# Performance work log

Hardware: AMD Instinct MI355X
Metric: run time of the kernel (lower is better)

The kernel has to match this reference:

```python
import jax, jax.numpy as jnp
import numpy as np

N = 65536          # number of active voxels
GRID = 96          # sparse volume side
P = 4              # cardinality (paths)
KS = 3             # kernel size per dim
K = KS ** 3        # 27 kernel offsets
DILS = [1, 3, 9, 27]
C_IN = 128
C_PATH = 32        # in/out features per path = 128 / 4
BN_EPS = 1e-5
LEAK = 0.0


def _build_kernel_maps():
    """Build padded gather/scatter maps per (path, kernel offset).

    in_map[p,k,:] / out_map[p,k,:]: out[out_idx] += W[k] @ x[in_idx].
    Padded with sentinel index N (maps to a zero row / dumped row).
    """
    rng = np.random.default_rng(0)
    flat = rng.choice(GRID ** 3, size=N, replace=False)
    coords = np.stack(np.unravel_index(flat, (GRID, GRID, GRID)), axis=1)  # [N,3]
    order = np.argsort(flat)
    sorted_keys = flat[order]
    offs = np.array([[dx, dy, dz] for dx in (-1, 0, 1)
                     for dy in (-1, 0, 1) for dz in (-1, 0, 1)])
    in_map = np.full((P, K, N), N, dtype=np.int32)
    out_map = np.full((P, K, N), N, dtype=np.int32)
    for p in range(P):
        d = DILS[p]
        for k in range(K):
            nb = coords + offs[k] * d
            valid = np.all((nb >= 0) & (nb < GRID), axis=1)
            nbkey = nb[:, 0] * GRID * GRID + nb[:, 1] * GRID + nb[:, 2]
            pos = np.clip(np.searchsorted(sorted_keys, nbkey), 0, N - 1)
            hit = valid & (sorted_keys[pos] == nbkey)
            j = np.nonzero(hit)[0]
            in_map[p, k, :j.size] = order[pos[j]].astype(np.int32)
            out_map[p, k, :j.size] = j.astype(np.int32)
    return jnp.asarray(in_map), jnp.asarray(out_map)


def setup_inputs() -> dict:
    key = jax.random.key(0)
    ks = jax.random.split(key, 4)
    in_map, out_map = _build_kernel_maps()
    return {
        "feats": jax.random.normal(ks[0], (N, C_IN), jnp.float32),
        "lin_W": jax.random.normal(ks[1], (P, C_IN, C_PATH), jnp.float32) * 0.05,
        "lin_b": jnp.zeros((P, C_PATH), jnp.float32),
        "conv_W": jax.random.normal(ks[2], (P, K, C_PATH, C_PATH), jnp.float32) * 0.05,
        "gamma": jnp.ones((P, C_PATH), jnp.float32),
        "beta": jnp.zeros((P, C_PATH), jnp.float32),
        "fin_W": jax.random.normal(ks[3], (C_IN, C_IN), jnp.float32) * 0.05,
        "fin_b": jnp.zeros((C_IN,), jnp.float32),
        "in_map": in_map,
        "out_map": out_map,
    }


def _sparse_conv(x, W, im, om):
    """x: [N,C]; W: [K,C,Co]; im/om: [K,N] padded index maps."""
    n = x.shape[0]
    co = W.shape[2]
    xp = jnp.concatenate([x, jnp.zeros((1, x.shape[1]), x.dtype)], axis=0)
    gathered = xp[im]                                   # [K,N,C]
    contrib = jnp.einsum('knc,kcd->knd', gathered, W)   # [K,N,Co]
    out = jnp.zeros((n + 1, co), x.dtype)
    out = out.at[om.reshape(-1)].add(contrib.reshape(-1, co))
    return out[:n]


def reference(feats, lin_W, lin_b, conv_W, gamma, beta, fin_W, fin_b,
              in_map, out_map):
    outs = []
    for p in range(P):
        h = feats @ lin_W[p] + lin_b[p]                 # MinkowskiLinear
        h = _sparse_conv(h, conv_W[p], in_map[p], out_map[p])
        mu = h.mean(axis=0)                             # BN (training stats)
        var = h.var(axis=0)
        h = (h - mu) * jax.lax.rsqrt(var + BN_EPS) * gamma[p] + beta[p]
        h = jax.nn.leaky_relu(h, LEAK)
        outs.append(h)
    cat = jnp.concatenate(outs, axis=1)                 # [N, 128]
    out = cat @ fin_W + fin_b + feats                   # linear + residual (identity)
    return out
```

## Files before the change

### kernel.cpp

```cpp
#include <hip/hip_runtime.h>


#define NN    65536
#define CIN   128
#define CPATH 32
#define NPATH 4
#define NK    27
#define TJ    512
#define NTILE (NN / TJ)
#define MAXG  288
#define SCALE_F 2097152.0f
#define INV_SCALE 4.76837158203125e-7f

typedef __attribute__((ext_vector_type(8))) short bfx8;
typedef __attribute__((ext_vector_type(4))) float fx4;

__device__ __forceinline__ unsigned short f2bf(float f) {
    unsigned u = __builtin_bit_cast(unsigned, f);
    u += 0x7FFFu + ((u >> 16) & 1u);
    return (unsigned short)(u >> 16);
}
__device__ __forceinline__ float bf2f(unsigned short s) {
    return __builtin_bit_cast(float, (unsigned)s << 16);
}
__device__ __forceinline__ bfx8 pack_bf8(const float4 a, const float4 b) {
    union { unsigned short s[8]; bfx8 v; } u;
    u.s[0] = f2bf(a.x); u.s[1] = f2bf(a.y); u.s[2] = f2bf(a.z); u.s[3] = f2bf(a.w);
    u.s[4] = f2bf(b.x); u.s[5] = f2bf(b.y); u.s[6] = f2bf(b.z); u.s[7] = f2bf(b.w);
    return u.v;
}

__global__ void wprep_rng(const float* __restrict__ convW,
                          const float* __restrict__ linW,
                          const float* __restrict__ finW,
                          const int* __restrict__ om,
                          unsigned short* __restrict__ Wt,
                          unsigned short* __restrict__ Wlt,
                          unsigned short* __restrict__ Wft,
                          unsigned short* __restrict__ Hb,
                          int* __restrict__ rngAll) {
    const int b = blockIdx.x;
    const int t = threadIdx.x;
    if (b < 108) {
        if (b == 0 && t < 64)
            ((unsigned*)(Hb + (size_t)NN * CIN))[t] = 0u;
        const int m = t >> 3;
        const int c0 = (t & 7) * 4;
        const float4 w = *(const float4*)(convW + ((size_t)b * CPATH + m) * CPATH + c0);
        unsigned short* o = Wt + (size_t)b * CPATH * CPATH;
        o[(c0 + 0) * CPATH + m] = f2bf(w.x);
        o[(c0 + 1) * CPATH + m] = f2bf(w.y);
        o[(c0 + 2) * CPATH + m] = f2bf(w.z);
        o[(c0 + 3) * CPATH + m] = f2bf(w.w);
    } else if (b < 112) {
        const int col = (b - 108) * 32 + (t >> 3);
        const int p = col >> 5, c = col & 31;
        const int k0 = (t & 7) * 16;
        for (int k = k0; k < k0 + 16; k++)
            Wlt[col * CIN + k] = f2bf(linW[(size_t)p * CIN * CPATH + k * CPATH + c]);
    } else if (b < 116) {
        const int col = (b - 112) * 32 + (t >> 3);
        const int k0 = (t & 7) * 16;
        for (int k = k0; k < k0 + 16; k++)
            Wft[col * CIN + k] = f2bf(finW[(size_t)k * CIN + col]);
    } else {
        const int idx = (b - 116) * 256 + t;
        if (idx < NPATH * NK * (NTILE + 1)) {
            const int tile = idx % (NTILE + 1);
            const int pk = idx / (NTILE + 1);
            const int bound = tile * TJ;
            const int* o = om + (size_t)pk * NN;
            int lo = 0, hi = NN;
            while (lo < hi) {
                const int mid = (lo + hi) >> 1;
                if (o[mid] < bound) lo = mid + 1; else hi = mid;
            }
            rngAll[idx] = lo;
        }
    }
}

__global__ void __launch_bounds__(256, 4)
lin_mfma(const float* __restrict__ feats,
         const unsigned short* __restrict__ Wlt,
         const float* __restrict__ linb,
         unsigned short* __restrict__ Hb) {
    const int tid = threadIdx.x;
    const int w = tid >> 6, lane = tid & 63;
    const int mrow = lane & 15, kq = lane >> 4;
    const int row = blockIdx.x * 64 + w * 16 + mrow;

    fx4 acc[8];
#pragma unroll
    for (int g = 0; g < 8; g++) acc[g] = (fx4){0.f, 0.f, 0.f, 0.f};

#pragma unroll
    for (int kt = 0; kt < 4; ++kt) {
        const float4 y0 = *(const float4*)(feats + (size_t)row * CIN + kt * 32 + kq * 8);
        const float4 y1 = *(const float4*)(feats + (size_t)row * CIN + kt * 32 + kq * 8 + 4);
        const bfx8 yf = pack_bf8(y0, y1);
#pragma unroll
        for (int g = 0; g < 8; g++) {
            const bfx8 xf = *(const bfx8*)(Wlt + (size_t)(g * 16 + mrow) * CIN + kt * 32 + kq * 8);
            acc[g] = __builtin_amdgcn_mfma_f32_16x16x32_bf16(xf, yf, acc[g], 0, 0, 0);
        }
    }
#pragma unroll
    for (int g = 0; g < 8; g++) {
        const int c0 = g * 16 + kq * 4;
        const float4 bb = *(const float4*)(linb + c0);
        union { unsigned short s[4]; ushort4 v; } u;
        u.s[0] = f2bf(acc[g][0] + bb.x);
        u.s[1] = f2bf(acc[g][1] + bb.y);
        u.s[2] = f2bf(acc[g][2] + bb.z);
        u.s[3] = f2bf(acc[g][3] + bb.w);
        *(ushort4*)(Hb + (size_t)row * CIN + c0) = u.v;
    }
}

__global__ void __launch_bounds__(512)
sconv12(const unsigned short* __restrict__ Hb,
        const unsigned short* __restrict__ Wt,
        const int* __restrict__ im,
        const int* __restrict__ om,
        const int* __restrict__ rngAll,
        unsigned short* __restrict__ Cbh,
        float* __restrict__ part) {
    __shared__ int accI[TJ + 1][33];
    __shared__ int rng[NK][2];
    __shared__ int gkA[MAXG], gtA[MAXG];
    __shared__ int gbase[NK];
    __shared__ int Gs;
    __shared__ float redS[16][32], redQ[16][32];

    const int p = blockIdx.y;
    const int T = blockIdx.x;
    const int j0 = T * TJ;
    const int tid = threadIdx.x;
    const int lane = tid & 63;
    const int w = tid >> 6;
    const int mrow = lane & 15, kq = lane >> 4;

    for (int idx = tid; idx < (TJ + 1) * 33; idx += 512)
        (&accI[0][0])[idx] = 0;
    if (tid < NK * 2) {
        const int k = tid >> 1, which = tid & 1;
        rng[k][which] = rngAll[((size_t)p * NK + k) * (NTILE + 1) + T + which];
    }
    __syncthreads();
    if (tid == 0) {
        int sum = 0;
#pragma unroll
        for (int k = 0; k < NK; k++) {
            gbase[k] = sum;
            sum += (rng[k][1] - rng[k][0] + 15) >> 4;
        }
        Gs = sum;
    }
    __syncthreads();
    if (tid < NK) {
        const int k = tid;
        const int s = rng[k][0];
        const int n = (rng[k][1] - s + 15) >> 4;
        const int b = gbase[k];
        for (int g = 0; g < n; g++) {
            gkA[b + g] = k;
            gtA[b + g] = s + g * 16;
        }
    }
    __syncthreads();

    const int G = Gs;
    const unsigned short* Wp = Wt + (size_t)p * NK * 1024 + kq * 8;
    const unsigned short* Hp = Hb + (size_t)p * CPATH + kq * 8;
    const int* omP = om + (size_t)p * NK * NN;
    const int* imP = im + (size_t)p * NK * NN;
    const fx4 z4 = {0.f, 0.f, 0.f, 0.f};

    for (int base = 2 * w; base < G; base += 16) {
        const int kA = gkA[base];
        const int tA = gtA[base] + mrow;
        int kB = 0, tB = NN + mrow;
        if (base + 1 < G) { kB = gkA[base + 1]; tB = gtA[base + 1] + mrow; }
        const int eA = rng[kA][1], eB = rng[kB][1];
        const bool vA = tA < eA, vB = tB < eB;
        const int jjA = vA ? (omP[(size_t)kA * NN + tA] - j0) : TJ;
        const int iA  = vA ? imP[(size_t)kA * NN + tA] : NN;
        const int jjB = vB ? (omP[(size_t)kB * NN + tB] - j0) : TJ;
        const int iB  = vB ? imP[(size_t)kB * NN + tB] : NN;
        const bfx8 xA0 = *(const bfx8*)(Wp + (size_t)kA * 1024 + mrow * CPATH);
        const bfx8 xA1 = *(const bfx8*)(Wp + (size_t)kA * 1024 + (16 + mrow) * CPATH);
        const bfx8 xB0 = *(const bfx8*)(Wp + (size_t)kB * 1024 + mrow * CPATH);
        const bfx8 xB1 = *(const bfx8*)(Wp + (size_t)kB * 1024 + (16 + mrow) * CPATH);
        const bfx8 yA = *(const bfx8*)(Hp + (size_t)iA * CIN);
        const bfx8 yB = *(const bfx8*)(Hp + (size_t)iB * CIN);
        const fx4 dA0 = __builtin_amdgcn_mfma_f32_16x16x32_bf16(xA0, yA, z4, 0, 0, 0);
        const fx4 dA1 = __builtin_amdgcn_mfma_f32_16x16x32_bf16(xA1, yA, z4, 0, 0, 0);
        const fx4 dB0 = __builtin_amdgcn_mfma_f32_16x16x32_bf16(xB0, yB, z4, 0, 0, 0);
        const fx4 dB1 = __builtin_amdgcn_mfma_f32_16x16x32_bf16(xB1, yB, z4, 0, 0, 0);
#pragma unroll
        for (int r = 0; r < 4; r++) {
            atomicAdd(&accI[jjA][kq * 4 + r],      (int)rintf(dA0[r] * SCALE_F));
            atomicAdd(&accI[jjA][16 + kq * 4 + r], (int)rintf(dA1[r] * SCALE_F));
            atomicAdd(&accI[jjB][kq * 4 + r],      (int)rintf(dB0[r] * SCALE_F));
            atomicAdd(&accI[jjB][16 + kq * 4 + r], (int)rintf(dB1[r] * SCALE_F));
        }
    }
    __syncthreads();

    {
        const int c = tid & 31;
        const int rg = tid >> 5;
        float s = 0.f, q = 0.f;
        for (int m = 0; m < TJ / 16; m++) {
            const int r = rg + 16 * m;
            const float f = (float)accI[r][c] * INV_SCALE;
            s += f;
            q = fmaf(f, f, q);
            Cbh[(size_t)(j0 + r) * CIN + p * CPATH + c] = f2bf(f);
        }
        redS[rg][c] = s;
        redQ[rg][c] = q;
    }
    __syncthreads();
    if (tid < 32) {
        float s = 0.f;
#pragma unroll
        for (int g = 0; g < 16; g++) s += redS[g][tid];
        part[(((size_t)p * NTILE) + T) * 64 + tid] = s;
    } else if (tid < 64) {
        const int c = tid - 32;
        float q = 0.f;
#pragma unroll
        for (int g = 0; g < 16; g++) q += redQ[g][c];
        part[(((size_t)p * NTILE) + T) * 64 + 32 + c] = q;
    }
}

__global__ void bn_stats2(const float* __restrict__ part,
                          const float* __restrict__ gamma,
                          const float* __restrict__ beta,
                          float* __restrict__ ss) {
    __shared__ float rs[4][128], rq[4][128];
    const int c = threadIdx.x & 127;
    const int ch = threadIdx.x >> 7;
    const int p = c >> 5, cc = c & 31;
    float s = 0.f, s2 = 0.f;
    for (int t = ch * (NTILE / 4); t < (ch + 1) * (NTILE / 4); t++) {
        s += part[(((size_t)p * NTILE) + t) * 64 + cc];
        s2 += part[(((size_t)p * NTILE) + t) * 64 + 32 + cc];
    }
    rs[ch][c] = s;
    rq[ch][c] = s2;
    __syncthreads();
    if (ch == 0) {
        s = rs[0][c] + rs[1][c] + rs[2][c] + rs[3][c];
        s2 = rq[0][c] + rq[1][c] + rq[2][c] + rq[3][c];
        const float mean = s * (1.f / NN);
        const float var = s2 * (1.f / NN) - mean * mean;
        const float sc = gamma[c] * rsqrtf(var + 1e-5f);
        ss[c] = sc;
        ss[128 + c] = beta[c] - mean * sc;
    }
}

__global__ void __launch_bounds__(256, 4)
fin_mfma(const unsigned short* __restrict__ Cbh,
         const float* __restrict__ ss,
         const unsigned short* __restrict__ Wft,
         const float* __restrict__ finb,
         const float* __restrict__ feats,
         float* __restrict__ out) {
    const int tid = threadIdx.x;
    const int w = tid >> 6, lane = tid & 63;
    const int mrow = lane & 15, kq = lane >> 4;
    const int row = blockIdx.x * 64 + w * 16 + mrow;

    fx4 acc[8];
#pragma unroll
    for (int g = 0; g < 8; g++) acc[g] = (fx4){0.f, 0.f, 0.f, 0.f};

#pragma unroll
    for (int kt = 0; kt < 4; ++kt) {
        const int k0 = kt * 32 + kq * 8;
        union { unsigned short s[8]; bfx8 v; } cb;
        cb.v = *(const bfx8*)(Cbh + (size_t)row * CIN + k0);
        const float4 sc0 = *(const float4*)(ss + k0);
        const float4 sc1 = *(const float4*)(ss + k0 + 4);
        const float4 sh0 = *(const float4*)(ss + 128 + k0);
        const float4 sh1 = *(const float4*)(ss + 128 + k0 + 4);
        float4 a, b;
        a.x = fmaxf(fmaf(bf2f(cb.s[0]), sc0.x, sh0.x), 0.f);
        a.y = fmaxf(fmaf(bf2f(cb.s[1]), sc0.y, sh0.y), 0.f);
        a.z = fmaxf(fmaf(bf2f(cb.s[2]), sc0.z, sh0.z), 0.f);
        a.w = fmaxf(fmaf(bf2f(cb.s[3]), sc0.w, sh0.w), 0.f);
        b.x = fmaxf(fmaf(bf2f(cb.s[4]), sc1.x, sh1.x), 0.f);
        b.y = fmaxf(fmaf(bf2f(cb.s[5]), sc1.y, sh1.y), 0.f);
        b.z = fmaxf(fmaf(bf2f(cb.s[6]), sc1.z, sh1.z), 0.f);
        b.w = fmaxf(fmaf(bf2f(cb.s[7]), sc1.w, sh1.w), 0.f);
        const bfx8 yf = pack_bf8(a, b);
#pragma unroll
        for (int g = 0; g < 8; g++) {
            const bfx8 xf = *(const bfx8*)(Wft + (size_t)(g * 16 + mrow) * CIN + kt * 32 + kq * 8);
            acc[g] = __builtin_amdgcn_mfma_f32_16x16x32_bf16(xf, yf, acc[g], 0, 0, 0);
        }
    }
#pragma unroll
    for (int g = 0; g < 8; g++) {
        const int c0 = g * 16 + kq * 4;
        const float4 fb = *(const float4*)(finb + c0);
        const float4 rs = *(const float4*)(feats + (size_t)row * CIN + c0);
        float4 o;
        o.x = acc[g][0] + fb.x + rs.x;
        o.y = acc[g][1] + fb.y + rs.y;
        o.z = acc[g][2] + fb.z + rs.z;
        o.w = acc[g][3] + fb.w + rs.w;
        *(float4*)(out + (size_t)row * CIN + c0) = o;
    }
}

extern "C" void kernel_launch(void* const* d_in, const int* in_sizes, int n_in,
                              void* d_out, int out_size, void* d_ws,
                              size_t ws_size, hipStream_t stream) {
    (void)in_sizes; (void)n_in; (void)out_size; (void)ws_size;
    const float* feats = (const float*)d_in[0];
    const float* linW  = (const float*)d_in[1];
    const float* linb  = (const float*)d_in[2];
    const float* convW = (const float*)d_in[3];
    const float* gamma = (const float*)d_in[4];
    const float* beta  = (const float*)d_in[5];
    const float* finW  = (const float*)d_in[6];
    const float* finb  = (const float*)d_in[7];
    const int*   im    = (const int*)d_in[8];
    const int*   om    = (const int*)d_in[9];
    float* out = (float*)d_out;

    char* ws = (char*)d_ws;
    unsigned short* Hb  = (unsigned short*)(ws);
    unsigned short* Cbh = (unsigned short*)(ws + 16781312);
    unsigned short* Wt  = (unsigned short*)(ws + 33558528);
    unsigned short* Wlt = (unsigned short*)(ws + 33779712);
    unsigned short* Wft = (unsigned short*)(ws + 33812480);
    int*   rngAll       = (int*)(ws + 33845248);
    float* part         = (float*)(ws + 33902592);
    float* ss           = (float*)(ws + 34033664);

    const int rng_total = NPATH * NK * (NTILE + 1);
    const int rng_blocks = (rng_total + 255) / 256;
    wprep_rng<<<116 + rng_blocks, 256, 0, stream>>>(convW, linW, finW, om,
                                                    Wt, Wlt, Wft, Hb, rngAll);
    lin_mfma<<<1024, 256, 0, stream>>>(feats, Wlt, linb, Hb);
    sconv12<<<dim3(NTILE, NPATH), 512, 0, stream>>>(Hb, Wt, im, om, rngAll, Cbh, part);
    bn_stats2<<<1, 512, 0, stream>>>(part, gamma, beta, ss);
    fin_mfma<<<1024, 256, 0, stream>>>(Cbh, ss, Wft, finb, feats, out);
}
```

Before: 93.68 us.

## Fuse all stages into one cooperative persistent kernel with grid syncs

Measured after the change: 327.5 us. +249.6%, slower.

```diff
diff --git a/kernel.cpp b/kernel.cpp
--- a/kernel.cpp
+++ b/kernel.cpp
@@ -1,4 +1,7 @@
 #include <hip/hip_runtime.h>
+#include <hip/hip_cooperative_groups.h>
+
+namespace cg = cooperative_groups;
 
 
 #define NN    65536
@@ -6,9 +9,9 @@
 #define CPATH 32
 #define NPATH 4
 #define NK    27
-#define TJ    512
+#define TJ    256
 #define NTILE (NN / TJ)
-#define MAXG  288
+#define MAXG  192
 #define SCALE_F 2097152.0f
 #define INV_SCALE 4.76837158203125e-7f
 
@@ -30,41 +33,36 @@
     return u.v;
 }
 
-__global__ void wprep_rng(const float* __restrict__ convW,
-                          const float* __restrict__ linW,
-                          const float* __restrict__ finW,
-                          const int* __restrict__ om,
-                          unsigned short* __restrict__ Wt,
-                          unsigned short* __restrict__ Wlt,
-                          unsigned short* __restrict__ Wft,
-                          unsigned short* __restrict__ Hb,
-                          int* __restrict__ rngAll) {
-    const int b = blockIdx.x;
-    const int t = threadIdx.x;
-    if (b < 108) {
-        if (b == 0 && t < 64)
-            ((unsigned*)(Hb + (size_t)NN * CIN))[t] = 0u;
-        const int m = t >> 3;
-        const int c0 = (t & 7) * 4;
-        const float4 w = *(const float4*)(convW + ((size_t)b * CPATH + m) * CPATH + c0);
-        unsigned short* o = Wt + (size_t)b * CPATH * CPATH;
-        o[(c0 + 0) * CPATH + m] = f2bf(w.x);
-        o[(c0 + 1) * CPATH + m] = f2bf(w.y);
-        o[(c0 + 2) * CPATH + m] = f2bf(w.z);
-        o[(c0 + 3) * CPATH + m] = f2bf(w.w);
-    } else if (b < 112) {
-        const int col = (b - 108) * 32 + (t >> 3);
+__device__ __forceinline__ void wprep_body(int vb, int vt,
+        const float* __restrict__ convW, const float* __restrict__ linW,
+        const float* __restrict__ finW, const int* __restrict__ om,
+        unsigned short* __restrict__ Wt, unsigned short* __restrict__ Wlt,
+        unsigned short* __restrict__ Wft, unsigned short* __restrict__ Hb,
+        int* __restrict__ rngAll) {
+    if (vb < 108) {
+        if (vb == 0 && vt < 64)
+            ((unsigned*)(Hb + (size_t)NN * CIN))[vt] = 0u;
+        const int m = vt >> 3;
+        const int c0 = (vt & 7) * 4;
+        const float4 wv = *(const float4*)(convW + ((size_t)vb * CPATH + m) * CPATH + c0);
+        unsigned short* o = Wt + (size_t)vb * CPATH * CPATH;
+        o[(c0 + 0) * CPATH + m] = f2bf(wv.x);
+        o[(c0 + 1) * CPATH + m] = f2bf(wv.y);
+        o[(c0 + 2) * CPATH + m] = f2bf(wv.z);
+        o[(c0 + 3) * CPATH + m] = f2bf(wv.w);
+    } else if (vb < 112) {
+        const int col = (vb - 108) * 32 + (vt >> 3);
         const int p = col >> 5, c = col & 31;
-        const int k0 = (t & 7) * 16;
+        const int k0 = (vt & 7) * 16;
         for (int k = k0; k < k0 + 16; k++)
             Wlt[col * CIN + k] = f2bf(linW[(size_t)p * CIN * CPATH + k * CPATH + c]);
-    } else if (b < 116) {
-        const int col = (b - 112) * 32 + (t >> 3);
-        const int k0 = (t & 7) * 16;
+    } else if (vb < 116) {
+        const int col = (vb - 112) * 32 + (vt >> 3);
+        const int k0 = (vt & 7) * 16;
         for (int k = k0; k < k0 + 16; k++)
             Wft[col * CIN + k] = f2bf(finW[(size_t)k * CIN + col]);
     } else {
-        const int idx = (b - 116) * 256 + t;
+        const int idx = (vb - 116) * 256 + vt;
         if (idx < NPATH * NK * (NTILE + 1)) {
             const int tile = idx % (NTILE + 1);
             const int pk = idx / (NTILE + 1);
@@ -80,20 +78,12 @@
     }
 }
 
-__global__ void __launch_bounds__(256, 4)
-lin_mfma(const float* __restrict__ feats,
-         const unsigned short* __restrict__ Wlt,
-         const float* __restrict__ linb,
-         unsigned short* __restrict__ Hb) {
-    const int tid = threadIdx.x;
-    const int w = tid >> 6, lane = tid & 63;
-    const int mrow = lane & 15, kq = lane >> 4;
-    const int row = blockIdx.x * 64 + w * 16 + mrow;
-
+__device__ __forceinline__ void lin_body(int row, int mrow, int kq,
+        const float* __restrict__ feats, const unsigned short* __restrict__ Wlt,
+        const float* __restrict__ linb, unsigned short* __restrict__ Hb) {
     fx4 acc[8];
 #pragma unroll
     for (int g = 0; g < 8; g++) acc[g] = (fx4){0.f, 0.f, 0.f, 0.f};
-
 #pragma unroll
     for (int kt = 0; kt < 4; ++kt) {
         const float4 y0 = *(const float4*)(feats + (size_t)row * CIN + kt * 32 + kq * 8);
@@ -118,168 +108,13 @@
     }
 }
 
-__global__ void __launch_bounds__(512)
-sconv12(const unsigned short* __restrict__ Hb,
-        const unsigned short* __restrict__ Wt,
-        const int* __restrict__ im,
-        const int* __restrict__ om,
-        const int* __restrict__ rngAll,
-        unsigned short* __restrict__ Cbh,
-        float* __restrict__ part) {
-    __shared__ int accI[TJ + 1][33];
-    __shared__ int rng[NK][2];
-    __shared__ int gkA[MAXG], gtA[MAXG];
-    __shared__ int gbase[NK];
-    __shared__ int Gs;
-    __shared__ float redS[16][32], redQ[16][32];
-
-    const int p = blockIdx.y;
-    const int T = blockIdx.x;
-    const int j0 = T * TJ;
-    const int tid = threadIdx.x;
-    const int lane = tid & 63;
-    const int w = tid >> 6;
-    const int mrow = lane & 15, kq = lane >> 4;
-
-    for (int idx = tid; idx < (TJ + 1) * 33; idx += 512)
-        (&accI[0][0])[idx] = 0;
-    if (tid < NK * 2) {
-        const int k = tid >> 1, which = tid & 1;
-        rng[k][which] = rngAll[((size_t)p * NK + k) * (NTILE + 1) + T + which];
-    }
-    __syncthreads();
-    if (tid == 0) {
-        int sum = 0;
-#pragma unroll
-        for (int k = 0; k < NK; k++) {
-            gbase[k] = sum;
-            sum += (rng[k][1] - rng[k][0] + 15) >> 4;
-        }
-        Gs = sum;
-    }
-    __syncthreads();
-    if (tid < NK) {
-        const int k = tid;
-        const int s = rng[k][0];
-        const int n = (rng[k][1] - s + 15) >> 4;
-        const int b = gbase[k];
-        for (int g = 0; g < n; g++) {
-            gkA[b + g] = k;
-            gtA[b + g] = s + g * 16;
-        }
-    }
-    __syncthreads();
-
-    const int G = Gs;
-    const unsigned short* Wp = Wt + (size_t)p * NK * 1024 + kq * 8;
-    const unsigned short* Hp = Hb + (size_t)p * CPATH + kq * 8;
-    const int* omP = om + (size_t)p * NK * NN;
-    const int* imP = im + (size_t)p * NK * NN;
-    const fx4 z4 = {0.f, 0.f, 0.f, 0.f};
-
-    for (int base = 2 * w; base < G; base += 16) {
-        const int kA = gkA[base];
-        const int tA = gtA[base] + mrow;
-        int kB = 0, tB = NN + mrow;
-        if (base + 1 < G) { kB = gkA[base + 1]; tB = gtA[base + 1] + mrow; }
-        const int eA = rng[kA][1], eB = rng[kB][1];
-        const bool vA = tA < eA, vB = tB < eB;
-        const int jjA = vA ? (omP[(size_t)kA * NN + tA] - j0) : TJ;
-        const int iA  = vA ? imP[(size_t)kA * NN + tA] : NN;
-        const int jjB = vB ? (omP[(size_t)kB * NN + tB] - j0) : TJ;
-        const int iB  = vB ? imP[(size_t)kB * NN + tB] : NN;
-        const bfx8 xA0 = *(const bfx8*)(Wp + (size_t)kA * 1024 + mrow * CPATH);
-        const bfx8 xA1 = *(const bfx8*)(Wp + (size_t)kA * 1024 + (16 + mrow) * CPATH);
-        const bfx8 xB0 = *(const bfx8*)(Wp + (size_t)kB * 1024 + mrow * CPATH);
-        const bfx8 xB1 = *(const bfx8*)(Wp + (size_t)kB * 1024 + (16 + mrow) * CPATH);
-        const bfx8 yA = *(const bfx8*)(Hp + (size_t)iA * CIN);
-        const bfx8 yB = *(const bfx8*)(Hp + (size_t)iB * CIN);
-        const fx4 dA0 = __builtin_amdgcn_mfma_f32_16x16x32_bf16(xA0, yA, z4, 0, 0, 0);
-        const fx4 dA1 = __builtin_amdgcn_mfma_f32_16x16x32_bf16(xA1, yA, z4, 0, 0, 0);
-        const fx4 dB0 = __builtin_amdgcn_mfma_f32_16x16x32_bf16(xB0, yB, z4, 0, 0, 0);
-        const fx4 dB1 = __builtin_amdgcn_mfma_f32_16x16x32_bf16(xB1, yB, z4, 0, 0, 0);
-#pragma unroll
-        for (int r = 0; r < 4; r++) {
-            atomicAdd(&accI[jjA][kq * 4 + r],      (int)rintf(dA0[r] * SCALE_F));
-            atomicAdd(&accI[jjA][16 + kq * 4 + r], (int)rintf(dA1[r] * SCALE_F));
-            atomicAdd(&accI[jjB][kq * 4 + r],      (int)rintf(dB0[r] * SCALE_F));
-            atomicAdd(&accI[jjB][16 + kq * 4 + r], (int)rintf(dB1[r] * SCALE_F));
-        }
-    }
-    __syncthreads();
-
-    {
-        const int c = tid & 31;
-        const int rg = tid >> 5;
-        float s = 0.f, q = 0.f;
-        for (int m = 0; m < TJ / 16; m++) {
-            const int r = rg + 16 * m;
-            const float f = (float)accI[r][c] * INV_SCALE;
-            s += f;
-            q = fmaf(f, f, q);
-            Cbh[(size_t)(j0 + r) * CIN + p * CPATH + c] = f2bf(f);
-        }
-        redS[rg][c] = s;
-        redQ[rg][c] = q;
-    }
-    __syncthreads();
-    if (tid < 32) {
-        float s = 0.f;
-#pragma unroll
-        for (int g = 0; g < 16; g++) s += redS[g][tid];
-        part[(((size_t)p * NTILE) + T) * 64 + tid] = s;
-    } else if (tid < 64) {
-        const int c = tid - 32;
-        float q = 0.f;
-#pragma unroll
-        for (int g = 0; g < 16; g++) q += redQ[g][c];
-        part[(((size_t)p * NTILE) + T) * 64 + 32 + c] = q;
-    }
-}
-
-__global__ void bn_stats2(const float* __restrict__ part,
-                          const float* __restrict__ gamma,
-                          const float* __restrict__ beta,
-                          float* __restrict__ ss) {
-    __shared__ float rs[4][128], rq[4][128];
-    const int c = threadIdx.x & 127;
-    const int ch = threadIdx.x >> 7;
-    const int p = c >> 5, cc = c & 31;
-    float s = 0.f, s2 = 0.f;
-    for (int t = ch * (NTILE / 4); t < (ch + 1) * (NTILE / 4); t++) {
-        s += part[(((size_t)p * NTILE) + t) * 64 + cc];
-        s2 += part[(((size_t)p * NTILE) + t) * 64 + 32 + cc];
-    }
-    rs[ch][c] = s;
-    rq[ch][c] = s2;
-    __syncthreads();
-    if (ch == 0) {
-        s = rs[0][c] + rs[1][c] + rs[2][c] + rs[3][c];
-        s2 = rq[0][c] + rq[1][c] + rq[2][c] + rq[3][c];
-        const float mean = s * (1.f / NN);
-        const float var = s2 * (1.f / NN) - mean * mean;
-        const float sc = gamma[c] * rsqrtf(var + 1e-5f);
-        ss[c] = sc;
-        ss[128 + c] = beta[c] - mean * sc;
-    }
-}
-
-__global__ void __launch_bounds__(256, 4)
-fin_mfma(const unsigned short* __restrict__ Cbh,
-         const float* __restrict__ ss,
-         const unsigned short* __restrict__ Wft,
-         const float* __restrict__ finb,
-         const float* __restrict__ feats,
-         float* __restrict__ out) {
-    const int tid = threadIdx.x;
-    const int w = tid >> 6, lane = tid & 63;
-    const int mrow = lane & 15, kq = lane >> 4;
-    const int row = blockIdx.x * 64 + w * 16 + mrow;
-
+__device__ __forceinline__ void fin_body(int row, int mrow, int kq,
+        const unsigned short* __restrict__ Cbh, const float* __restrict__ ss,
+        const unsigned short* __restrict__ Wft, const float* __restrict__ finb,
+        const float* __restrict__ feats, float* __restrict__ out) {
     fx4 acc[8];
 #pragma unroll
     for (int g = 0; g < 8; g++) acc[g] = (fx4){0.f, 0.f, 0.f, 0.f};
-
 #pragma unroll
     for (int kt = 0; kt < 4; ++kt) {
         const int k0 = kt * 32 + kq * 8;
@@ -289,16 +124,16 @@
         const float4 sc1 = *(const float4*)(ss + k0 + 4);
         const float4 sh0 = *(const float4*)(ss + 128 + k0);
         const float4 sh1 = *(const float4*)(ss + 128 + k0 + 4);
-        float4 a, b;
+        float4 a, bb;
         a.x = fmaxf(fmaf(bf2f(cb.s[0]), sc0.x, sh0.x), 0.f);
         a.y = fmaxf(fmaf(bf2f(cb.s[1]), sc0.y, sh0.y), 0.f);
         a.z = fmaxf(fmaf(bf2f(cb.s[2]), sc0.z, sh0.z), 0.f);
         a.w = fmaxf(fmaf(bf2f(cb.s[3]), sc0.w, sh0.w), 0.f);
-        b.x = fmaxf(fmaf(bf2f(cb.s[4]), sc1.x, sh1.x), 0.f);
-        b.y = fmaxf(fmaf(bf2f(cb.s[5]), sc1.y, sh1.y), 0.f);
-        b.z = fmaxf(fmaf(bf2f(cb.s[6]), sc1.z, sh1.z), 0.f);
-        b.w = fmaxf(fmaf(bf2f(cb.s[7]), sc1.w, sh1.w), 0.f);
-        const bfx8 yf = pack_bf8(a, b);
+        bb.x = fmaxf(fmaf(bf2f(cb.s[4]), sc1.x, sh1.x), 0.f);
+        bb.y = fmaxf(fmaf(bf2f(cb.s[5]), sc1.y, sh1.y), 0.f);
+        bb.z = fmaxf(fmaf(bf2f(cb.s[6]), sc1.z, sh1.z), 0.f);
+        bb.w = fmaxf(fmaf(bf2f(cb.s[7]), sc1.w, sh1.w), 0.f);
+        const bfx8 yf = pack_bf8(a, bb);
 #pragma unroll
         for (int g = 0; g < 8; g++) {
             const bfx8 xf = *(const bfx8*)(Wft + (size_t)(g * 16 + mrow) * CIN + kt * 32 + kq * 8);
@@ -317,6 +152,271 @@
         o.w = acc[g][3] + fb.w + rs.w;
         *(float4*)(out + (size_t)row * CIN + c0) = o;
     }
+}
+
+struct SconvLds {
+    int accI[TJ + 1][33];
+    int rng[NK][2];
+    int gk[MAXG], gt[MAXG];
+    int gbase[NK];
+    int Gs;
+    float redS[32][32], redQ[32][32];
+};
+
+__device__ __forceinline__ void sconv_body(SconvLds* sh, int p, int T,
+        int tid, int w, int mrow, int kq,
+        const unsigned short* __restrict__ Hb, const unsigned short* __restrict__ Wt,
+        const int* __restrict__ im, const int* __restrict__ om,
+        const int* __restrict__ rngAll, unsigned short* __restrict__ Cbh,
+        float* __restrict__ part) {
+    const int j0 = T * TJ;
+    for (int idx = tid; idx < (TJ + 1) * 33; idx += 512)
+        (&sh->accI[0][0])[idx] = 0;
+    if (tid < NK * 2) {
+        const int k = tid >> 1, which = tid & 1;
+        sh->rng[k][which] = rngAll[((size_t)p * NK + k) * (NTILE + 1) + T + which];
+    }
+    __syncthreads();
+    if (tid == 0) {
+        int sum = 0;
+#pragma unroll
+        for (int k = 0; k < NK; k++) {
+            sh->gbase[k] = sum;
+            if (k != 13)
+                sum += (sh->rng[k][1] - sh->rng[k][0] + 15) >> 4;
+        }
+        sh->Gs = sum;
+    }
+    __syncthreads();
+    if (tid < NK && tid != 13) {
+        const int k = tid;
+        const int s = sh->rng[k][0];
+        const int n = (sh->rng[k][1] - s + 15) >> 4;
+        const int bb = sh->gbase[k];
+        for (int g = 0; g < n; g++) {
+            sh->gk[bb + g] = k;
+            sh->gt[bb + g] = s + g * 16;
+        }
+    }
+    __syncthreads();
+
+    const int G = sh->Gs;
+    const unsigned short* Wp = Wt + (size_t)p * NK * 1024 + kq * 8;
+    const unsigned short* Hp = Hb + (size_t)p * CPATH + kq * 8;
+    const int* omP = om + (size_t)p * NK * NN;
+    const int* imP = im + (size_t)p * NK * NN;
+    const fx4 z4 = {0.f, 0.f, 0.f, 0.f};
+
+    {
+        const bfx8 xc0 = *(const bfx8*)(Wp + (size_t)13 * 1024 + mrow * CPATH);
+        const bfx8 xc1 = *(const bfx8*)(Wp + (size_t)13 * 1024 + (16 + mrow) * CPATH);
+        const int r0 = w * 32 + mrow;
+        const bfx8 yc0 = *(const bfx8*)(Hp + (size_t)(j0 + r0     ) * CIN);
+        const bfx8 yc1 = *(const bfx8*)(Hp + (size_t)(j0 + r0 + 16) * CIN);
+        const fx4 e00 = __builtin_amdgcn_mfma_f32_16x16x32_bf16(xc0, yc0, z4, 0, 0, 0);
+        const fx4 e01 = __builtin_amdgcn_mfma_f32_16x16x32_bf16(xc1, yc0, z4, 0, 0, 0);
+        const fx4 e10 = __builtin_amdgcn_mfma_f32_16x16x32_bf16(xc0, yc1, z4, 0, 0, 0);
+        const fx4 e11 = __builtin_amdgcn_mfma_f32_16x16x32_bf16(xc1, yc1, z4, 0, 0, 0);
+#pragma unroll
+        for (int r = 0; r < 4; r++) {
+            atomicAdd(&sh->accI[r0     ][kq * 4 + r],      (int)rintf(e00[r] * SCALE_F));
+            atomicAdd(&sh->accI[r0     ][16 + kq * 4 + r], (int)rintf(e01[r] * SCALE_F));
+            atomicAdd(&sh->accI[r0 + 16][kq * 4 + r],      (int)rintf(e10[r] * SCALE_F));
+            atomicAdd(&sh->accI[r0 + 16][16 + kq * 4 + r], (int)rintf(e11[r] * SCALE_F));
+        }
+    }
+
+    for (int base = 2 * w; base < G; base += 16) {
+        const int kA = sh->gk[base];
+        const int tA = sh->gt[base] + mrow;
+        int kB = 0, tB = NN + mrow;
+        if (base + 1 < G) { kB = sh->gk[base + 1]; tB = sh->gt[base + 1] + mrow; }
+        const bool vA = tA < sh->rng[kA][1], vB = tB < sh->rng[kB][1];
+        const int jjA = vA ? (omP[(size_t)kA * NN + tA] - j0) : TJ;
+        const int iA  = vA ? imP[(size_t)kA * NN + tA] : NN;
+        const int jjB = vB ? (omP[(size_t)kB * NN + tB] - j0) : TJ;
+        const int iB  = vB ? imP[(size_t)kB * NN + tB] : NN;
+        const bfx8 yA = *(const bfx8*)(Hp + (size_t)iA * CIN);
+        const bfx8 yB = *(const bfx8*)(Hp + (size_t)iB * CIN);
+        const bfx8 xa0 = *(const bfx8*)(Wp + (size_t)kA * 1024 + mrow * CPATH);
+        const bfx8 xb0 = *(const bfx8*)(Wp + (size_t)kA * 1024 + (16 + mrow) * CPATH);
+        const bfx8 xa1 = *(const bfx8*)(Wp + (size_t)kB * 1024 + mrow * CPATH);
+        const bfx8 xb1 = *(const bfx8*)(Wp + (size_t)kB * 1024 + (16 + mrow) * CPATH);
+        const fx4 dA0 = __builtin_amdgcn_mfma_f32_16x16x32_bf16(xa0, yA, z4, 0, 0, 0);
+        const fx4 dA1 = __builtin_amdgcn_mfma_f32_16x16x32_bf16(xb0, yA, z4, 0, 0, 0);
+        const fx4 dB0 = __builtin_amdgcn_mfma_f32_16x16x32_bf16(xa1, yB, z4, 0, 0, 0);
+        const fx4 dB1 = __builtin_amdgcn_mfma_f32_16x16x32_bf16(xb1, yB, z4, 0, 0, 0);
+#pragma unroll
+        for (int r = 0; r < 4; r++) {
+            atomicAdd(&sh->accI[jjA][kq * 4 + r],      (int)rintf(dA0[r] * SCALE_F));
+            atomicAdd(&sh->accI[jjA][16 + kq * 4 + r], (int)rintf(dA1[r] * SCALE_F));
+            atomicAdd(&sh->accI[jjB][kq * 4 + r],      (int)rintf(dB0[r] * SCALE_F));
+            atomicAdd(&sh->accI[jjB][16 + kq * 4 + r], (int)rintf(dB1[r] * SCALE_F));
+        }
+    }
+    __syncthreads();
+
+    {
+        const int c0 = (tid & 15) * 2;
+        const int rg = tid >> 4;
+        float s0 = 0.f, q0 = 0.f, s1 = 0.f, q1 = 0.f;
+        for (int m = 0; m < 8; m++) {
+            const int r = rg + 32 * m;
+            const float f0 = (float)sh->accI[r][c0] * INV_SCALE;
+            const float f1 = (float)sh->accI[r][c0 + 1] * INV_SCALE;
+            s0 += f0; q0 = fmaf(f0, f0, q0);
+            s1 += f1; q1 = fmaf(f1, f1, q1);
+            const unsigned pk2 = (unsigned)f2bf(f0) | ((unsigned)f2bf(f1) << 16);
+            *(unsigned*)(Cbh + (size_t)(j0 + r) * CIN + p * CPATH + c0) = pk2;
+        }
+        sh->redS[rg][c0] = s0; sh->redS[rg][c0 + 1] = s1;
+        sh->redQ[rg][c0] = q0; sh->redQ[rg][c0 + 1] = q1;
+    }
+    __syncthreads();
+    if (tid < 32) {
+        float s = 0.f;
+#pragma unroll
+        for (int g = 0; g < 32; g++) s += sh->redS[g][tid];
+        part[(((size_t)p * NTILE) + T) * 64 + tid] = s;
+    } else if (tid < 64) {
+        const int c = tid - 32;
+        float q = 0.f;
+#pragma unroll
+        for (int g = 0; g < 32; g++) q += sh->redQ[g][c];
+        part[(((size_t)p * NTILE) + T) * 64 + 32 + c] = q;
+    }
+}
+
+__global__ void __launch_bounds__(512, 4)
+fused(const float* __restrict__ feats, const float* __restrict__ linW,
+      const float* __restrict__ linb, const float* __restrict__ convW,
+      const float* __restrict__ gamma, const float* __restrict__ beta,
+      const float* __restrict__ finW, const float* __restrict__ finb,
+      const int* __restrict__ im, const int* __restrict__ om,
+      float* __restrict__ out,
+      unsigned short* __restrict__ Hb, unsigned short* __restrict__ Cbh,
+      unsigned short* __restrict__ Wt, unsigned short* __restrict__ Wlt,
+      unsigned short* __restrict__ Wft, int* __restrict__ rngAll,
+      float* __restrict__ part, float* __restrict__ ss) {
+    cg::grid_group grid = cg::this_grid();
+
+    __shared__ union {
+        SconvLds s2;
+        struct { float rs[4][128], rq[4][128]; } s3;
+    } sh;
+
+    const int b = blockIdx.x;
+    const int tid = threadIdx.x;
+    const int lane = tid & 63;
+    const int w = tid >> 6;
+    const int mrow = lane & 15, kq = lane >> 4;
+
+    {
+        const int g = b * 512 + tid;
+        wprep_body(g >> 8, g & 255, convW, linW, finW, om, Wt, Wlt, Wft, Hb, rngAll);
+    }
+    grid.sync();
+
+    lin_body(b * 128 + w * 16 + mrow, mrow, kq, feats, Wlt, linb, Hb);
+    grid.sync();
+
+    for (int it = 0; it < 2; ++it) {
+        const int pair = b + it * 512;
+        sconv_body(&sh.s2, pair >> 8, pair & 255, tid, w, mrow, kq,
+                   Hb, Wt, im, om, rngAll, Cbh, part);
+        __syncthreads();
+    }
+    grid.sync();
+
+    if (b == 0) {
+        const int c = tid & 127;
+        const int ch = tid >> 7;
+        const int p = c >> 5, cc = c & 31;
+        float s = 0.f, s2 = 0.f;
+        for (int t = ch * (NTILE / 4); t < (ch + 1) * (NTILE / 4); t++) {
+            s += part[(((size_t)p * NTILE) + t) * 64 + cc];
+            s2 += part[(((size_t)p * NTILE) + t) * 64 + 32 + cc];
+        }
+        sh.s3.rs[ch][c] = s;
+        sh.s3.rq[ch][c] = s2;
+        __syncthreads();
+        if (ch == 0) {
+            s = sh.s3.rs[0][c] + sh.s3.rs[1][c] + sh.s3.rs[2][c] + sh.s3.rs[3][c];
+            s2 = sh.s3.rq[0][c] + sh.s3.rq[1][c] + sh.s3.rq[2][c] + sh.s3.rq[3][c];
+            const float mean = s * (1.f / NN);
+            const float var = s2 * (1.f / NN) - mean * mean;
+            const float sc = gamma[c] * rsqrtf(var + 1e-5f);
+            ss[c] = sc;
+            ss[128 + c] = beta[c] - mean * sc;
+        }
+    }
+    grid.sync();
+
+    fin_body(b * 128 + w * 16 + mrow, mrow, kq, Cbh, ss, Wft, finb, feats, out);
+}
+
+__global__ void wprep_k(const float* __restrict__ convW, const float* __restrict__ linW,
+                        const float* __restrict__ finW, const int* __restrict__ om,
+                        unsigned short* __restrict__ Wt, unsigned short* __restrict__ Wlt,
+                        unsigned short* __restrict__ Wft, unsigned short* __restrict__ Hb,
+                        int* __restrict__ rngAll) {
+    wprep_body(blockIdx.x, threadIdx.x, convW, linW, finW, om, Wt, Wlt, Wft, Hb, rngAll);
+}
+
+__global__ void __launch_bounds__(256, 4)
+lin_k(const float* __restrict__ feats, const unsigned short* __restrict__ Wlt,
+      const float* __restrict__ linb, unsigned short* __restrict__ Hb) {
+    const int tid = threadIdx.x;
+    const int lane = tid & 63;
+    lin_body(blockIdx.x * 64 + (tid >> 6) * 16 + (lane & 15), lane & 15, lane >> 4,
+             feats, Wlt, linb, Hb);
+}
+
+__global__ void __launch_bounds__(512)
+sconv_k(const unsigned short* __restrict__ Hb, const unsigned short* __restrict__ Wt,
+        const int* __restrict__ im, const int* __restrict__ om,
+        const int* __restrict__ rngAll, unsigned short* __restrict__ Cbh,
+        float* __restrict__ part) {
+    __shared__ SconvLds sh;
+    const int tid = threadIdx.x;
+    const int lane = tid & 63;
+    sconv_body(&sh, blockIdx.y, blockIdx.x, tid, tid >> 6, lane & 15, lane >> 4,
+               Hb, Wt, im, om, rngAll, Cbh, part);
+}
+
+__global__ void bn_k(const float* __restrict__ part, const float* __restrict__ gamma,
+                     const float* __restrict__ beta, float* __restrict__ ss) {
+    __shared__ float rs[4][128], rq[4][128];
+    const int c = threadIdx.x & 127;
+    const int ch = threadIdx.x >> 7;
+    const int p = c >> 5, cc = c & 31;
+    float s = 0.f, s2 = 0.f;
+    for (int t = ch * (NTILE / 4); t < (ch + 1) * (NTILE / 4); t++) {
+        s += part[(((size_t)p * NTILE) + t) * 64 + cc];
+        s2 += part[(((size_t)p * NTILE) + t) * 64 + 32 + cc];
+    }
+    rs[ch][c] = s;
+    rq[ch][c] = s2;
+    __syncthreads();
+    if (ch == 0) {
+        s = rs[0][c] + rs[1][c] + rs[2][c] + rs[3][c];
+        s2 = rq[0][c] + rq[1][c] + rq[2][c] + rq[3][c];
+        const float mean = s * (1.f / NN);
+        const float var = s2 * (1.f / NN) - mean * mean;
+        const float sc = gamma[c] * rsqrtf(var + 1e-5f);
+        ss[c] = sc;
+        ss[128 + c] = beta[c] - mean * sc;
+    }
+}
+
+__global__ void __launch_bounds__(256, 4)
+fin_k(const unsigned short* __restrict__ Cbh, const float* __restrict__ ss,
+      const unsigned short* __restrict__ Wft, const float* __restrict__ finb,
+      const float* __restrict__ feats, float* __restrict__ out) {
+    const int tid = threadIdx.x;
+    const int lane = tid & 63;
+    fin_body(blockIdx.x * 64 + (tid >> 6) * 16 + (lane & 15), lane & 15, lane >> 4,
+             Cbh, ss, Wft, finb, feats, out);
 }
 
 extern "C" void kernel_launch(void* const* d_in, const int* in_sizes, int n_in,
@@ -342,15 +442,26 @@
     unsigned short* Wlt = (unsigned short*)(ws + 33779712);
     unsigned short* Wft = (unsigned short*)(ws + 33812480);
     int*   rngAll       = (int*)(ws + 33845248);
-    float* part         = (float*)(ws + 33902592);
-    float* ss           = (float*)(ws + 34033664);
-
-    const int rng_total = NPATH * NK * (NTILE + 1);
-    const int rng_blocks = (rng_total + 255) / 256;
-    wprep_rng<<<116 + rng_blocks, 256, 0, stream>>>(convW, linW, finW, om,
-                                                    Wt, Wlt, Wft, Hb, rngAll);
-    lin_mfma<<<1024, 256, 0, stream>>>(feats, Wlt, linb, Hb);
-    sconv12<<<dim3(NTILE, NPATH), 512, 0, stream>>>(Hb, Wt, im, om, rngAll, Cbh, part);
-    bn_stats2<<<1, 512, 0, stream>>>(part, gamma, beta, ss);
-    fin_mfma<<<1024, 256, 0, stream>>>(Cbh, ss, Wft, finb, feats, out);
-}
+    float* part         = (float*)(ws + 33959936);
+    float* ss           = (float*)(ws + 34222080);
+
+    void* args[] = {
+        (void*)&feats, (void*)&linW, (void*)&linb, (void*)&convW,
+        (void*)&gamma, (void*)&beta, (void*)&finW, (void*)&finb,
+        (void*)&im, (void*)&om, (void*)&out,
+        (void*)&Hb, (void*)&Cbh, (void*)&Wt, (void*)&Wlt, (void*)&Wft,
+        (void*)&rngAll, (void*)&part, (void*)&ss
+    };
+    hipError_t err = hipLaunchCooperativeKernel((const void*)fused, dim3(512),
+                                                dim3(512), args, 0, stream);
+    if (err != hipSuccess) {
+        const int rng_total = NPATH * NK * (NTILE + 1);
+        const int rng_blocks = (rng_total + 255) / 256;
+        wprep_k<<<116 + rng_blocks, 256, 0, stream>>>(convW, linW, finW, om,
+                                                      Wt, Wlt, Wft, Hb, rngAll);
+        lin_k<<<1024, 256, 0, stream>>>(feats, Wlt, linb, Hb);
+        sconv_k<<<dim3(NTILE, NPATH), 512, 0, stream>>>(Hb, Wt, im, om, rngAll, Cbh, part);
+        bn_k<<<1, 512, 0, stream>>>(part, gamma, beta, ss);
+        fin_k<<<1024, 256, 0, stream>>>(Cbh, ss, Wft, finb, feats, out);
+    }
+}
```
